# Kernel tuning notes

Hardware: AMD Instinct MI355X
Metric: run time of the kernel (lower is better)

Reference implementation:

```python
import jax, jax.numpy as jnp
import numpy as np
from jax import lax

NL = 2        # num mamba layers
D_MODEL = 200
D_STATE = 16
D_CONV = 4
DI = 400      # expand * d_model
DT_RANK = 13  # ceil(d_model / 16)
B = 256
L = 256
EPS = 1e-12


def _ln(x, w, b):
    mu = jnp.mean(x, axis=-1, keepdims=True)
    var = jnp.mean((x - mu) ** 2, axis=-1, keepdims=True)
    return (x - mu) / jnp.sqrt(var + EPS) * w + b


def _mamba(x, in_proj_w, conv_w, conv_b, x_proj_w, dt_proj_w, dt_proj_b, A_log, D, out_proj_w):
    b, l, _ = x.shape
    xz = jnp.einsum('bld,ed->ble', x, in_proj_w)  # [b,l,2*DI]
    xc, z = jnp.split(xz, 2, axis=-1)
    # causal depthwise conv over time (pad d_conv-1 on the left == pytorch pad+slice)
    xt = xc.transpose(0, 2, 1)  # [b,DI,l]
    xt = lax.conv_general_dilated(xt, conv_w[:, None, :], (1,), [(D_CONV - 1, 0)],
                                  dimension_numbers=('NCH', 'OIH', 'NCH'),
                                  feature_group_count=DI)
    xc = jax.nn.silu(xt + conv_b[None, :, None]).transpose(0, 2, 1)  # [b,l,DI]
    x_dbl = jnp.einsum('bld,ed->ble', xc, x_proj_w)  # [b,l,DT_RANK+2*N]
    dt = x_dbl[..., :DT_RANK]
    Bm = x_dbl[..., DT_RANK:DT_RANK + D_STATE]
    Cm = x_dbl[..., DT_RANK + D_STATE:]
    delta = jax.nn.softplus(jnp.einsum('blr,dr->bld', dt, dt_proj_w) + dt_proj_b)  # [b,l,DI]
    A = -jnp.exp(A_log)  # [DI,N]

    def step(h, inp):
        d_t, u_t, B_t, C_t = inp  # [b,DI],[b,DI],[b,N],[b,N]
        dA = jnp.exp(d_t[..., None] * A)  # [b,DI,N]
        h = dA * h + (d_t * u_t)[..., None] * B_t[:, None, :]
        y = jnp.einsum('bdn,bn->bd', h, C_t)
        return h, y

    h0 = jnp.zeros((b, DI, D_STATE), dtype=x.dtype)
    xs = (delta.transpose(1, 0, 2), xc.transpose(1, 0, 2),
          Bm.transpose(1, 0, 2), Cm.transpose(1, 0, 2))
    _, ys = lax.scan(step, h0, xs)
    y = ys.transpose(1, 0, 2) + xc * D  # [b,l,DI]
    y = y * jax.nn.silu(z)
    return jnp.einsum('bld,ed->ble', y, out_proj_w)


def _forward(item_emb, in_proj_w, conv_w, conv_b, x_proj_w, dt_proj_w, dt_proj_b,
             A_log, D, out_proj_w, ln1_w, ln1_b, ffn_w1, ffn_b1, ffn_w2, ffn_b2,
             ffn_ln_w, ffn_ln_b):
    h = item_emb
    for i in range(NL):
        m = _mamba(h, in_proj_w[i], conv_w[i], conv_b[i], x_proj_w[i],
                   dt_proj_w[i], dt_proj_b[i], A_log[i], D[i], out_proj_w[i])
        h = _ln(m + h, ln1_w[i], ln1_b[i])  # num_layers > 1 -> residual branch
        f = jnp.einsum('bld,ed->ble', h, ffn_w1[i]) + ffn_b1[i]
        f = jax.nn.gelu(f, approximate=False)  # torch nn.GELU default = exact
        f = jnp.einsum('ble,de->bld', f, ffn_w2[i]) + ffn_b2[i]
        h = _ln(f + h, ffn_ln_w[i], ffn_ln_b[i])
    c = h[:, -1:, :]
    x_n = h[:, :-1, :]
    return c, x_n


def setup_inputs() -> dict:
    key = jax.random.key(0)
    ks = jax.random.split(key, 10)
    s = 0.02
    f32 = jnp.float32
    A_log = jnp.broadcast_to(jnp.log(jnp.arange(1, D_STATE + 1, dtype=f32)),
                             (NL, DI, D_STATE))
    return {
        'item_emb': jax.random.normal(ks[0], (B, L, D_MODEL), f32),
        'item_seq_len': jax.random.randint(ks[1], (B,), 1, L, jnp.int32),
        'in_proj_w': s * jax.random.normal(ks[2], (NL, 2 * DI, D_MODEL), f32),
        'conv_w': s * jax.random.normal(ks[3], (NL, DI, D_CONV), f32),
        'conv_b': jnp.zeros((NL, DI), f32),
        'x_proj_w': s * jax.random.normal(ks[4], (NL, DT_RANK + 2 * D_STATE, DI), f32),
        'dt_proj_w': s * jax.random.normal(ks[5], (NL, DI, DT_RANK), f32),
        'dt_proj_b': s * jax.random.normal(ks[6], (NL, DI), f32),
        'A_log': A_log,
        'D': jnp.ones((NL, DI), f32),
        'out_proj_w': s * jax.random.normal(ks[7], (NL, D_MODEL, DI), f32),
        'ln1_w': jnp.ones((NL, D_MODEL), f32),
        'ln1_b': jnp.zeros((NL, D_MODEL), f32),
        'ffn_w1': s * jax.random.normal(ks[8], (NL, 4 * D_MODEL, D_MODEL), f32),
        'ffn_b1': jnp.zeros((NL, 4 * D_MODEL), f32),
        'ffn_w2': s * jax.random.normal(ks[9], (NL, D_MODEL, 4 * D_MODEL), f32),
        'ffn_b2': jnp.zeros((NL, D_MODEL), f32),
        'ffn_ln_w': jnp.ones((NL, D_MODEL), f32),
        'ffn_ln_b': jnp.zeros((NL, D_MODEL), f32),
    }


def reference(item_emb, item_seq_len, in_proj_w, conv_w, conv_b, x_proj_w,
              dt_proj_w, dt_proj_b, A_log, D, out_proj_w, ln1_w, ln1_b,
              ffn_w1, ffn_b1, ffn_w2, ffn_b2, ffn_ln_w, ffn_ln_b):
    # item_seq_len is accepted but unused by Mamba4Rec.forward
    return _forward(item_emb, in_proj_w, conv_w, conv_b, x_proj_w, dt_proj_w,
                    dt_proj_b, A_log, D, out_proj_w, ln1_w, ln1_b, ffn_w1,
                    ffn_b1, ffn_w2, ffn_b2, ffn_ln_w, ffn_ln_b)
```

## Files before the change

kernel.cpp:

```cpp
#include <hip/hip_runtime.h>
#include <hip/hip_bf16.h>

#define DM 200
#define DIE 400
#define LSEQ 256
#define NB 256

typedef __hip_bfloat16 bf16;
typedef const float* fp;
typedef __attribute__((ext_vector_type(8))) short short8;
typedef __attribute__((ext_vector_type(4))) float f32x4;

__device__ __forceinline__ float b2f(bf16 x) { return __bfloat162float(x); }
__device__ __forceinline__ bf16  f2b(float x) { return __float2bfloat16(x); }

__device__ __forceinline__ unsigned short f2bbits(float f) {
    union { float f; unsigned int u; } c; c.f = f;
    unsigned int u = c.u;
    unsigned int r = (u + 0x7fffu + ((u >> 16) & 1u)) >> 16;
    return (unsigned short)r;
}
__device__ __forceinline__ unsigned short ldb(const float* p) { return f2bbits(*p); }
__device__ __forceinline__ unsigned short ldb(const bf16* p) { return *(const unsigned short*)p; }
__device__ __forceinline__ void stf(float* p, float v) { *p = v; }
__device__ __forceinline__ void stf(bf16* p, float v) { *p = f2b(v); }

template <typename TA, typename TC, int EPI>
__global__ __launch_bounds__(256) void gemm_mfma(const TA* __restrict__ A, int lda,
                                                 const float* __restrict__ W,
                                                 const float* __restrict__ bias,
                                                 TC* __restrict__ C, int ldc,
                                                 int N, int K) {
    constexpr int LS = 40;
    __shared__ short As[128 * LS];
    __shared__ short Bs[128 * LS];
    const int m0 = blockIdx.x * 128;
    const int n0 = blockIdx.y * 128;
    const int tid = threadIdx.x;
    const int wave = tid >> 6;
    const int lane = tid & 63;
    const int wm = (wave & 1) * 64;
    const int wn = (wave >> 1) * 64;
    const int fm = lane & 15;
    const int quad = lane >> 4;

    f32x4 acc[4][4] = {};

    const int sr = tid >> 1;
    const int sc = (tid & 1) * 16;

    for (int k0 = 0; k0 < K; k0 += 32) {
        {
            const TA* src = A + (size_t)(m0 + sr) * lda + k0 + sc;
            short* dst = As + sr * LS + sc;
            if (k0 + sc + 16 <= K) {
#pragma unroll
                for (int j = 0; j < 16; ++j) dst[j] = (short)ldb(src + j);
            } else {
#pragma unroll
                for (int j = 0; j < 16; ++j)
                    dst[j] = (k0 + sc + j < K) ? (short)ldb(src + j) : (short)0;
            }
        }
        {
            short* dst = Bs + sr * LS + sc;
            if (n0 + sr < N) {
                const float* src = W + (size_t)(n0 + sr) * K + k0 + sc;
                if (k0 + sc + 16 <= K) {
#pragma unroll
                    for (int j = 0; j < 16; ++j) dst[j] = (short)f2bbits(src[j]);
                } else {
#pragma unroll
                    for (int j = 0; j < 16; ++j)
                        dst[j] = (k0 + sc + j < K) ? (short)f2bbits(src[j]) : (short)0;
                }
            } else {
#pragma unroll
                for (int j = 0; j < 16; ++j) dst[j] = 0;
            }
        }
        __syncthreads();
        short8 af[4], bfr[4];
#pragma unroll
        for (int i = 0; i < 4; ++i)
            af[i] = *(const short8*)(As + (wm + i * 16 + fm) * LS + quad * 8);
#pragma unroll
        for (int j = 0; j < 4; ++j)
            bfr[j] = *(const short8*)(Bs + (wn + j * 16 + fm) * LS + quad * 8);
#pragma unroll
        for (int i = 0; i < 4; ++i)
#pragma unroll
            for (int j = 0; j < 4; ++j)
                acc[i][j] = __builtin_amdgcn_mfma_f32_16x16x32_bf16(af[i], bfr[j], acc[i][j], 0, 0, 0);
        __syncthreads();
    }

#pragma unroll
    for (int j = 0; j < 4; ++j) {
        int n = n0 + wn + j * 16 + fm;
        if (n >= N) continue;
        float bv = (EPI == 2 || EPI == 3) ? bias[n] : 0.f;
#pragma unroll
        for (int i = 0; i < 4; ++i) {
#pragma unroll
            for (int r = 0; r < 4; ++r) {
                int m = m0 + wm + i * 16 + quad * 4 + r;
                float v = acc[i][j][r];
                if (EPI == 2) {
                    v += bv;
                    v = 0.5f * v * (1.f + erff(v * 0.70710678118654752f));
                } else if (EPI == 3) {
                    v += bv;
                }
                stf(&C[(size_t)m * ldc + n], v);
            }
        }
    }
}

__global__ __launch_bounds__(256) void conv_silu_inplace(bf16* __restrict__ xz,
                                                         const float* __restrict__ cw,
                                                         const float* __restrict__ cb,
                                                         int total ) {
    int idx = blockIdx.x * 256 + threadIdx.x;
    if (idx >= total) return;
    int d = idx % DIE;
    int b = idx / DIE;
    float w0 = cw[d * 4 + 0];
    float w1 = cw[d * 4 + 1];
    float w2 = cw[d * 4 + 2];
    float w3 = cw[d * 4 + 3];
    float bias = cb[d];
    float x0 = 0.f, x1 = 0.f, x2 = 0.f;
    bf16* p = xz + (size_t)b * LSEQ * 800 + d;
    for (int t = 0; t < LSEQ; ++t) {
        float x = b2f(*p);
        float s = bias + w0 * x0 + w1 * x1 + w2 * x2 + w3 * x;
        x0 = x1; x1 = x2; x2 = x;
        float sig = __builtin_amdgcn_rcpf(1.f + __expf(-s));
        *p = f2b(s * sig);
        p += 800;
    }
}

__global__ __launch_bounds__(256) void scan_kernel(const float* __restrict__ xdbl,
                                                   bf16* __restrict__ xz,
                                                   const float* __restrict__ dt_w,
                                                   const float* __restrict__ dt_b,
                                                   const float* __restrict__ A_log,
                                                   const float* __restrict__ Dw) {
    const int b = blockIdx.x >> 1;
    const int half = blockIdx.x & 1;
    const int tid = threadIdx.x;
    if (tid >= 200) return;
    const int d = half * 200 + tid;

    float A2[16], Wr[13];
#pragma unroll
    for (int n = 0; n < 16; ++n) A2[n] = -__expf(A_log[d * 16 + n]);
#pragma unroll
    for (int r = 0; r < 13; ++r) Wr[r] = dt_w[d * 13 + r];
    const float bdt = dt_b[d];
    const float Dv = Dw[d];

    float h[16];
#pragma unroll
    for (int n = 0; n < 16; ++n) h[n] = 0.f;

    const float* __restrict__ rp = xdbl + (size_t)b * LSEQ * 45;
    bf16* __restrict__ xp = xz + (size_t)b * LSEQ * 800 + d;

    auto scan_step = [&](const float* cur, float ut, float zv, bf16* outp) {
        float dtv = bdt;
#pragma unroll
        for (int r = 0; r < 13; ++r) dtv += Wr[r] * cur[r];
        float sp = (dtv > 20.f) ? dtv : __logf(1.f + __expf(dtv));
        float du = sp * ut;
        float yv = 0.f;
#pragma unroll
        for (int n = 0; n < 16; ++n) {
            float dA = __expf(sp * A2[n]);
            h[n] = dA * h[n] + du * cur[13 + n];
            yv += h[n] * cur[29 + n];
        }
        yv += ut * Dv;
        float sig = __builtin_amdgcn_rcpf(1.f + __expf(-zv));
        *outp = f2b(yv * zv * sig);
    };

    float ca[45], cbuf[45];
#pragma unroll
    for (int j = 0; j < 45; ++j) ca[j] = rp[j];
    float utA = b2f(xp[0]);
    float zvA = b2f(xp[400]);

    for (int t = 0; t < LSEQ; t += 2) {
#pragma unroll
        for (int j = 0; j < 45; ++j) cbuf[j] = rp[45 + j];
        float utB = b2f(xp[800]);
        float zvB = b2f(xp[1200]);

        scan_step(ca, utA, zvA, xp);

        if (t + 2 < LSEQ) {
#pragma unroll
            for (int j = 0; j < 45; ++j) ca[j] = rp[90 + j];
            utA = b2f(xp[1600]);
            zvA = b2f(xp[2000]);
        }

        scan_step(cbuf, utB, zvB, xp + 800);

        rp += 90;
        xp += 1600;
    }
}

__global__ __launch_bounds__(256) void ln_res_kernel(const float* __restrict__ xa,
                                                     const float* __restrict__ xb,
                                                     const float* __restrict__ w,
                                                     const float* __restrict__ bias,
                                                     float* __restrict__ dst, int rows) {
    int wave = threadIdx.x >> 6;
    int lane = threadIdx.x & 63;
    int row = blockIdx.x * 4 + wave;
    if (row >= rows) return;
    const float* pa = xa + (size_t)row * DM;
    const float* pb = xb + (size_t)row * DM;
    float v[4];
    float sum = 0.f, sq = 0.f;
#pragma unroll
    for (int i = 0; i < 4; ++i) {
        int c = lane + i * 64;
        float t = 0.f;
        if (c < DM) t = pa[c] + pb[c];
        v[i] = t;
        sum += t;
        sq += t * t;
    }
#pragma unroll
    for (int off = 32; off > 0; off >>= 1) {
        sum += __shfl_down(sum, off);
        sq += __shfl_down(sq, off);
    }
    sum = __shfl(sum, 0);
    sq = __shfl(sq, 0);
    float mu = sum * (1.f / DM);
    float var = fmaxf(sq * (1.f / DM) - mu * mu, 0.f);
    float rstd = rsqrtf(var + 1e-12f);
    float* pd = dst + (size_t)row * DM;
#pragma unroll
    for (int i = 0; i < 4; ++i) {
        int c = lane + i * 64;
        if (c < DM) pd[c] = (v[i] - mu) * rstd * w[c] + bias[c];
    }
}

__global__ __launch_bounds__(256) void write_out_kernel(const float* __restrict__ h,
                                                        float* __restrict__ out,
                                                        int b0, int total ) {
    int idx = blockIdx.x * 256 + threadIdx.x;
    if (idx >= total) return;
    int d = idx % DM;
    int bl = idx / DM;
    int l = bl % LSEQ;
    int b = b0 + bl / LSEQ;
    float v = h[idx];
    if (l == LSEQ - 1) {
        out[b * DM + d] = v;
    } else {
        out[(size_t)NB * DM + ((size_t)(b * (LSEQ - 1) + l) * DM + d)] = v;
    }
}

extern "C" void kernel_launch(void* const* d_in, const int* in_sizes, int n_in,
                              void* d_out, int out_size, void* d_ws, size_t ws_size,
                              hipStream_t stream) {
    fp emb       = (fp)d_in[0];
    fp in_proj_w = (fp)d_in[2];
    fp conv_w    = (fp)d_in[3];
    fp conv_b    = (fp)d_in[4];
    fp x_proj_w  = (fp)d_in[5];
    fp dt_proj_w = (fp)d_in[6];
    fp dt_proj_b = (fp)d_in[7];
    fp A_log     = (fp)d_in[8];
    fp Dw        = (fp)d_in[9];
    fp out_proj_w= (fp)d_in[10];
    fp ln1_w     = (fp)d_in[11];
    fp ln1_b     = (fp)d_in[12];
    fp ffn_w1    = (fp)d_in[13];
    fp ffn_b1    = (fp)d_in[14];
    fp ffn_w2    = (fp)d_in[15];
    fp ffn_b2    = (fp)d_in[16];
    fp ffn_ln_w  = (fp)d_in[17];
    fp ffn_ln_b  = (fp)d_in[18];

    const int cands[8] = {256, 128, 64, 32, 16, 8, 4, 2};
    int cb = 2;
    for (int ci = 0; ci < 8; ++ci) {
        size_t rcx = (size_t)cands[ci] * LSEQ;
        if (rcx * 3380 <= ws_size) { cb = cands[ci]; break; }
    }
    const size_t rc = (size_t)cb * LSEQ;

    bf16*  xz   = (bf16*)d_ws;
    float* xdbl = (float*)(xz + rc * 800);
    float* m    = xdbl + rc * 45;
    float* h    = m + rc * 200;

    const int rcDM = (int)rc * DM;
    const int gm = (int)rc / 128;

    for (int b0 = 0; b0 < NB; b0 += cb) {
        const float* emb_chunk = emb + (size_t)b0 * LSEQ * DM;

        for (int i = 0; i < 2; ++i) {
            fp w_in  = in_proj_w + (size_t)i * 800 * 200;
            fp cw    = conv_w + (size_t)i * 400 * 4;
            fp cbp   = conv_b + (size_t)i * 400;
            fp w_xp  = x_proj_w + (size_t)i * 45 * 400;
            fp w_dt  = dt_proj_w + (size_t)i * 400 * 13;
            fp b_dt  = dt_proj_b + (size_t)i * 400;
            fp Ai    = A_log + (size_t)i * 400 * 16;
            fp Di    = Dw + (size_t)i * 400;
            fp w_op  = out_proj_w + (size_t)i * 200 * 400;
            fp l1w   = ln1_w + (size_t)i * 200;
            fp l1b   = ln1_b + (size_t)i * 200;
            fp f1w   = ffn_w1 + (size_t)i * 800 * 200;
            fp f1b   = ffn_b1 + (size_t)i * 800;
            fp f2w   = ffn_w2 + (size_t)i * 200 * 800;
            fp f2b_  = ffn_b2 + (size_t)i * 200;
            fp flw   = ffn_ln_w + (size_t)i * 200;
            fp flb   = ffn_ln_b + (size_t)i * 200;

            const float* hin = (i == 0) ? emb_chunk : h;

            gemm_mfma<float, bf16, 0><<<dim3(gm, 7), 256, 0, stream>>>(
                hin, 200, w_in, nullptr, xz, 800, 800, 200);
            conv_silu_inplace<<<(cb * DIE + 255) / 256, 256, 0, stream>>>(xz, cw, cbp, cb * DIE);
            gemm_mfma<bf16, float, 0><<<dim3(gm, 1), 256, 0, stream>>>(
                xz, 800, w_xp, nullptr, xdbl, 45, 45, 400);
            scan_kernel<<<cb * 2, 256, 0, stream>>>(xdbl, xz, w_dt, b_dt, Ai, Di);
            gemm_mfma<bf16, float, 0><<<dim3(gm, 2), 256, 0, stream>>>(
                xz, 800, w_op, nullptr, m, 200, 200, 400);
            ln_res_kernel<<<rc / 4, 256, 0, stream>>>(m, hin, l1w, l1b, h, (int)rc);
            gemm_mfma<float, bf16, 2><<<dim3(gm, 7), 256, 0, stream>>>(
                h, 200, f1w, f1b, xz, 800, 800, 200);
            gemm_mfma<bf16, float, 3><<<dim3(gm, 2), 256, 0, stream>>>(
                xz, 800, f2w, f2b_, m, 200, 200, 800);
            ln_res_kernel<<<rc / 4, 256, 0, stream>>>(m, h, flw, flb, h, (int)rc);
        }

        write_out_kernel<<<rcDM / 256, 256, 0, stream>>>(h, (float*)d_out, b0, rcDM);
    }
}
```

Baseline: 1.480 ms.

## Pre-convert weights and activations to bf16, vectorize GEMM loads, use power-chain dA in scan

Weights are converted to bf16 once per call into workspace, and the layer-norm kernels also write a bf16 copy of the hidden state, so GEMM tile loads become vectorized 16-byte bf16 copies instead of per-element float-to-bf16 conversions. The scan kernel checks at runtime whether A equals -(n+1) (the standard S4D init) and, if so, computes the 16 decay factors as powers of a single exp instead of 16 exps. The extra conversion kernels and bf16 stores add some memory traffic. The fast scan path relies on the A_log initialisation matching the test inputs, though a generic fallback is kept.

```diff
diff --git a/kernel.cpp b/kernel.cpp
--- a/kernel.cpp
+++ b/kernel.cpp
@@ -9,6 +9,7 @@
 typedef __hip_bfloat16 bf16;
 typedef const float* fp;
 typedef __attribute__((ext_vector_type(8))) short short8;
+typedef __attribute__((ext_vector_type(4))) short short4_t;
 typedef __attribute__((ext_vector_type(4))) float f32x4;
 
 __device__ __forceinline__ float b2f(bf16 x) { return __bfloat162float(x); }
@@ -20,14 +21,50 @@
     unsigned int r = (u + 0x7fffu + ((u >> 16) & 1u)) >> 16;
     return (unsigned short)r;
 }
-__device__ __forceinline__ unsigned short ldb(const float* p) { return f2bbits(*p); }
-__device__ __forceinline__ unsigned short ldb(const bf16* p) { return *(const unsigned short*)p; }
 __device__ __forceinline__ void stf(float* p, float v) { *p = v; }
 __device__ __forceinline__ void stf(bf16* p, float v) { *p = f2b(v); }
 
-template <typename TA, typename TC, int EPI>
-__global__ __launch_bounds__(256) void gemm_mfma(const TA* __restrict__ A, int lda,
-                                                 const float* __restrict__ W,
+#define W_XP_OFF 320000
+#define W_OP_OFF 356000
+#define W_F1_OFF 516000
+#define W_F2_OFF 836000
+#define W_TOTAL  1156000
+#define W_BYTES  2312000
+
+__global__ __launch_bounds__(256) void wcvt_kernel(fp a0, fp a1, fp a2, fp a3, fp a4,
+                                                   bf16* __restrict__ dst) {
+    int g = blockIdx.x * 256 + threadIdx.x;
+    if (g >= W_TOTAL / 4) return;
+    int idx = g * 4;
+    const float* src;
+    int off;
+    if (idx < W_XP_OFF)      { src = a0; off = idx; }
+    else if (idx < W_OP_OFF) { src = a1; off = idx - W_XP_OFF; }
+    else if (idx < W_F1_OFF) { src = a2; off = idx - W_OP_OFF; }
+    else if (idx < W_F2_OFF) { src = a3; off = idx - W_F1_OFF; }
+    else                     { src = a4; off = idx - W_F2_OFF; }
+    float4 v = *(const float4*)(src + off);
+    short4_t o;
+    o.x = (short)f2bbits(v.x); o.y = (short)f2bbits(v.y);
+    o.z = (short)f2bbits(v.z); o.w = (short)f2bbits(v.w);
+    *(short4_t*)((short*)dst + idx) = o;
+}
+
+__global__ __launch_bounds__(256) void cvt_kernel(const float* __restrict__ src,
+                                                  bf16* __restrict__ dst, int n4) {
+    int g = blockIdx.x * 256 + threadIdx.x;
+    if (g >= n4) return;
+    int idx = g * 4;
+    float4 v = *(const float4*)(src + idx);
+    short4_t o;
+    o.x = (short)f2bbits(v.x); o.y = (short)f2bbits(v.y);
+    o.z = (short)f2bbits(v.z); o.w = (short)f2bbits(v.w);
+    *(short4_t*)((short*)dst + idx) = o;
+}
+
+template <typename TC, int EPI>
+__global__ __launch_bounds__(256) void gemm_mfma(const bf16* __restrict__ A, int lda,
+                                                 const bf16* __restrict__ W,
                                                  const float* __restrict__ bias,
                                                  TC* __restrict__ C, int ldc,
                                                  int N, int K) {
@@ -51,28 +88,28 @@
 
     for (int k0 = 0; k0 < K; k0 += 32) {
         {
-            const TA* src = A + (size_t)(m0 + sr) * lda + k0 + sc;
+            const short* src = (const short*)A + (size_t)(m0 + sr) * lda + k0 + sc;
             short* dst = As + sr * LS + sc;
             if (k0 + sc + 16 <= K) {
-#pragma unroll
-                for (int j = 0; j < 16; ++j) dst[j] = (short)ldb(src + j);
+                *(short8*)dst = *(const short8*)src;
+                *(short8*)(dst + 8) = *(const short8*)(src + 8);
             } else {
 #pragma unroll
                 for (int j = 0; j < 16; ++j)
-                    dst[j] = (k0 + sc + j < K) ? (short)ldb(src + j) : (short)0;
+                    dst[j] = (k0 + sc + j < K) ? src[j] : (short)0;
             }
         }
         {
             short* dst = Bs + sr * LS + sc;
             if (n0 + sr < N) {
-                const float* src = W + (size_t)(n0 + sr) * K + k0 + sc;
+                const short* src = (const short*)W + (size_t)(n0 + sr) * K + k0 + sc;
                 if (k0 + sc + 16 <= K) {
-#pragma unroll
-                    for (int j = 0; j < 16; ++j) dst[j] = (short)f2bbits(src[j]);
+                    *(short8*)dst = *(const short8*)src;
+                    *(short8*)(dst + 8) = *(const short8*)(src + 8);
                 } else {
 #pragma unroll
                     for (int j = 0; j < 16; ++j)
-                        dst[j] = (k0 + sc + j < K) ? (short)f2bbits(src[j]) : (short)0;
+                        dst[j] = (k0 + sc + j < K) ? src[j] : (short)0;
                 }
             } else {
 #pragma unroll
@@ -143,6 +180,73 @@
     }
 }
 
+template <bool FAST>
+__device__ __forceinline__ void scan_body(const float* __restrict__ rp,
+                                          bf16* __restrict__ xp,
+                                          const float* Wr, const float* A2,
+                                          float bdt, float Dv) {
+    float h[16];
+#pragma unroll
+    for (int n = 0; n < 16; ++n) h[n] = 0.f;
+
+    auto scan_step = [&](const float* cur, float ut, float zv, bf16* outp) {
+        float dtv = bdt;
+#pragma unroll
+        for (int r = 0; r < 13; ++r) dtv += Wr[r] * cur[r];
+        float sp = (dtv > 20.f) ? dtv : __logf(1.f + __expf(dtv));
+        float du = sp * ut;
+        float dA[16];
+        if (FAST) {
+            float r1 = __expf(-sp);
+            float r2 = r1 * r1, r3 = r2 * r1, r4 = r2 * r2;
+            float r5 = r4 * r1, r6 = r4 * r2, r7 = r4 * r3, r8 = r4 * r4;
+            dA[0] = r1;  dA[1] = r2;  dA[2] = r3;  dA[3] = r4;
+            dA[4] = r5;  dA[5] = r6;  dA[6] = r7;  dA[7] = r8;
+            dA[8] = r8 * r1;  dA[9] = r8 * r2;  dA[10] = r8 * r3;  dA[11] = r8 * r4;
+            dA[12] = r8 * r5; dA[13] = r8 * r6; dA[14] = r8 * r7;  dA[15] = r8 * r8;
+        } else {
+#pragma unroll
+            for (int n = 0; n < 16; ++n) dA[n] = __expf(sp * A2[n]);
+        }
+        float yv = 0.f;
+#pragma unroll
+        for (int n = 0; n < 16; ++n) {
+            h[n] = dA[n] * h[n] + du * cur[13 + n];
+            yv += h[n] * cur[29 + n];
+        }
+        yv += ut * Dv;
+        float sig = __builtin_amdgcn_rcpf(1.f + __expf(-zv));
+        *outp = f2b(yv * zv * sig);
+    };
+
+    float ca[45], cbuf[45];
+#pragma unroll
+    for (int j = 0; j < 45; ++j) ca[j] = rp[j];
+    float utA = b2f(xp[0]);
+    float zvA = b2f(xp[400]);
+
+    for (int t = 0; t < LSEQ; t += 2) {
+#pragma unroll
+        for (int j = 0; j < 45; ++j) cbuf[j] = rp[45 + j];
+        float utB = b2f(xp[800]);
+        float zvB = b2f(xp[1200]);
+
+        scan_step(ca, utA, zvA, xp);
+
+        if (t + 2 < LSEQ) {
+#pragma unroll
+            for (int j = 0; j < 45; ++j) ca[j] = rp[90 + j];
+            utA = b2f(xp[1600]);
+            zvA = b2f(xp[2000]);
+        }
+
+        scan_step(cbuf, utB, zvB, xp + 800);
+
+        rp += 90;
+        xp += 1600;
+    }
+}
+
 __global__ __launch_bounds__(256) void scan_kernel(const float* __restrict__ xdbl,
                                                    bf16* __restrict__ xz,
                                                    const float* __restrict__ dt_w,
@@ -156,71 +260,30 @@
     const int d = half * 200 + tid;
 
     float A2[16], Wr[13];
-#pragma unroll
-    for (int n = 0; n < 16; ++n) A2[n] = -__expf(A_log[d * 16 + n]);
+    bool fast = true;
+#pragma unroll
+    for (int n = 0; n < 16; ++n) {
+        A2[n] = -__expf(A_log[d * 16 + n]);
+        fast = fast && (fabsf(A2[n] + (float)(n + 1)) < 1e-3f);
+    }
 #pragma unroll
     for (int r = 0; r < 13; ++r) Wr[r] = dt_w[d * 13 + r];
     const float bdt = dt_b[d];
     const float Dv = Dw[d];
 
-    float h[16];
-#pragma unroll
-    for (int n = 0; n < 16; ++n) h[n] = 0.f;
-
     const float* __restrict__ rp = xdbl + (size_t)b * LSEQ * 45;
     bf16* __restrict__ xp = xz + (size_t)b * LSEQ * 800 + d;
 
-    auto scan_step = [&](const float* cur, float ut, float zv, bf16* outp) {
-        float dtv = bdt;
-#pragma unroll
-        for (int r = 0; r < 13; ++r) dtv += Wr[r] * cur[r];
-        float sp = (dtv > 20.f) ? dtv : __logf(1.f + __expf(dtv));
-        float du = sp * ut;
-        float yv = 0.f;
-#pragma unroll
-        for (int n = 0; n < 16; ++n) {
-            float dA = __expf(sp * A2[n]);
-            h[n] = dA * h[n] + du * cur[13 + n];
-            yv += h[n] * cur[29 + n];
-        }
-        yv += ut * Dv;
-        float sig = __builtin_amdgcn_rcpf(1.f + __expf(-zv));
-        *outp = f2b(yv * zv * sig);
-    };
-
-    float ca[45], cbuf[45];
-#pragma unroll
-    for (int j = 0; j < 45; ++j) ca[j] = rp[j];
-    float utA = b2f(xp[0]);
-    float zvA = b2f(xp[400]);
-
-    for (int t = 0; t < LSEQ; t += 2) {
-#pragma unroll
-        for (int j = 0; j < 45; ++j) cbuf[j] = rp[45 + j];
-        float utB = b2f(xp[800]);
-        float zvB = b2f(xp[1200]);
-
-        scan_step(ca, utA, zvA, xp);
-
-        if (t + 2 < LSEQ) {
-#pragma unroll
-            for (int j = 0; j < 45; ++j) ca[j] = rp[90 + j];
-            utA = b2f(xp[1600]);
-            zvA = b2f(xp[2000]);
-        }
-
-        scan_step(cbuf, utB, zvB, xp + 800);
-
-        rp += 90;
-        xp += 1600;
-    }
+    if (fast) scan_body<true>(rp, xp, Wr, A2, bdt, Dv);
+    else      scan_body<false>(rp, xp, Wr, A2, bdt, Dv);
 }
 
 __global__ __launch_bounds__(256) void ln_res_kernel(const float* __restrict__ xa,
-                                                     const float* __restrict__ xb,
+                                                     const float* xb,
                                                      const float* __restrict__ w,
                                                      const float* __restrict__ bias,
-                                                     float* __restrict__ dst, int rows) {
+                                                     float* dst,
+                                                     bf16* __restrict__ dstb, int rows) {
     int wave = threadIdx.x >> 6;
     int lane = threadIdx.x & 63;
     int row = blockIdx.x * 4 + wave;
@@ -249,10 +312,15 @@
     float var = fmaxf(sq * (1.f / DM) - mu * mu, 0.f);
     float rstd = rsqrtf(var + 1e-12f);
     float* pd = dst + (size_t)row * DM;
+    bf16* pdb = dstb + (size_t)row * DM;
 #pragma unroll
     for (int i = 0; i < 4; ++i) {
         int c = lane + i * 64;
-        if (c < DM) pd[c] = (v[i] - mu) * rstd * w[c] + bias[c];
+        if (c < DM) {
+            float o = (v[i] - mu) * rstd * w[c] + bias[c];
+            pd[c] = o;
+            pdb[c] = f2b(o);
+        }
     }
 }
 
@@ -299,56 +367,63 @@
     int cb = 2;
     for (int ci = 0; ci < 8; ++ci) {
         size_t rcx = (size_t)cands[ci] * LSEQ;
-        if (rcx * 3380 <= ws_size) { cb = cands[ci]; break; }
+        if (rcx * 3780 + W_BYTES + 1024 <= ws_size) { cb = cands[ci]; break; }
     }
     const size_t rc = (size_t)cb * LSEQ;
 
-    bf16*  xz   = (bf16*)d_ws;
-    float* xdbl = (float*)(xz + rc * 800);
+    bf16*  wb   = (bf16*)d_ws;
+    bf16*  xz   = (bf16*)((char*)d_ws + W_BYTES);
+    bf16*  hb   = xz + rc * 800;
+    float* xdbl = (float*)(hb + rc * 200);
     float* m    = xdbl + rc * 45;
     float* h    = m + rc * 200;
 
+    wcvt_kernel<<<(W_TOTAL / 4 + 255) / 256, 256, 0, stream>>>(
+        in_proj_w, x_proj_w, out_proj_w, ffn_w1, ffn_w2, wb);
+
     const int rcDM = (int)rc * DM;
     const int gm = (int)rc / 128;
 
     for (int b0 = 0; b0 < NB; b0 += cb) {
         const float* emb_chunk = emb + (size_t)b0 * LSEQ * DM;
 
+        cvt_kernel<<<(rcDM / 4 + 255) / 256, 256, 0, stream>>>(emb_chunk, hb, rcDM / 4);
+
         for (int i = 0; i < 2; ++i) {
-            fp w_in  = in_proj_w + (size_t)i * 800 * 200;
+            const bf16* wb_in = wb + (size_t)i * 160000;
+            const bf16* wb_xp = wb + W_XP_OFF + (size_t)i * 18000;
+            const bf16* wb_op = wb + W_OP_OFF + (size_t)i * 80000;
+            const bf16* wb_f1 = wb + W_F1_OFF + (size_t)i * 160000;
+            const bf16* wb_f2 = wb + W_F2_OFF + (size_t)i * 160000;
             fp cw    = conv_w + (size_t)i * 400 * 4;
             fp cbp   = conv_b + (size_t)i * 400;
-            fp w_xp  = x_proj_w + (size_t)i * 45 * 400;
             fp w_dt  = dt_proj_w + (size_t)i * 400 * 13;
             fp b_dt  = dt_proj_b + (size_t)i * 400;
             fp Ai    = A_log + (size_t)i * 400 * 16;
             fp Di    = Dw + (size_t)i * 400;
-            fp w_op  = out_proj_w + (size_t)i * 200 * 400;
             fp l1w   = ln1_w + (size_t)i * 200;
             fp l1b   = ln1_b + (size_t)i * 200;
-            fp f1w   = ffn_w1 + (size_t)i * 800 * 200;
             fp f1b   = ffn_b1 + (size_t)i * 800;
-            fp f2w   = ffn_w2 + (size_t)i * 200 * 800;
             fp f2b_  = ffn_b2 + (size_t)i * 200;
             fp flw   = ffn_ln_w + (size_t)i * 200;
             fp flb   = ffn_ln_b + (size_t)i * 200;
 
             const float* hin = (i == 0) ? emb_chunk : h;
 
-            gemm_mfma<float, bf16, 0><<<dim3(gm, 7), 256, 0, stream>>>(
-                hin, 200, w_in, nullptr, xz, 800, 800, 200);
+            gemm_mfma<bf16, 0><<<dim3(gm, 7), 256, 0, stream>>>(
+                hb, 200, wb_in, nullptr, xz, 800, 800, 200);
             conv_silu_inplace<<<(cb * DIE + 255) / 256, 256, 0, stream>>>(xz, cw, cbp, cb * DIE);
-            gemm_mfma<bf16, float, 0><<<dim3(gm, 1), 256, 0, stream>>>(
-                xz, 800, w_xp, nullptr, xdbl, 45, 45, 400);
+            gemm_mfma<float, 0><<<dim3(gm, 1), 256, 0, stream>>>(
+                xz, 800, wb_xp, nullptr, xdbl, 45, 45, 400);
             scan_kernel<<<cb * 2, 256, 0, stream>>>(xdbl, xz, w_dt, b_dt, Ai, Di);
-            gemm_mfma<bf16, float, 0><<<dim3(gm, 2), 256, 0, stream>>>(
-                xz, 800, w_op, nullptr, m, 200, 200, 400);
-            ln_res_kernel<<<rc / 4, 256, 0, stream>>>(m, hin, l1w, l1b, h, (int)rc);
-            gemm_mfma<float, bf16, 2><<<dim3(gm, 7), 256, 0, stream>>>(
-                h, 200, f1w, f1b, xz, 800, 800, 200);
-            gemm_mfma<bf16, float, 3><<<dim3(gm, 2), 256, 0, stream>>>(
-                xz, 800, f2w, f2b_, m, 200, 200, 800);
-            ln_res_kernel<<<rc / 4, 256, 0, stream>>>(m, h, flw, flb, h, (int)rc);
+            gemm_mfma<float, 0><<<dim3(gm, 2), 256, 0, stream>>>(
+                xz, 800, wb_op, nullptr, m, 200, 200, 400);
+            ln_res_kernel<<<rc / 4, 256, 0, stream>>>(m, hin, l1w, l1b, h, hb, (int)rc);
+            gemm_mfma<bf16, 2><<<dim3(gm, 7), 256, 0, stream>>>(
+                hb, 200, wb_f1, f1b, xz, 800, 800, 200);
+            gemm_mfma<float, 3><<<dim3(gm, 2), 256, 0, stream>>>(
+                xz, 800, wb_f2, f2b_, m, 200, 200, 800);
+            ln_res_kernel<<<rc / 4, 256, 0, stream>>>(m, h, flw, flb, h, hb, (int)rc);
         }
 
         write_out_kernel<<<rcDM / 256, 256, 0, stream>>>(h, (float*)d_out, b0, rcDM);
```

Measured after the change: 1.306 ms. 11.8% less time.
